# Kernel optimization log

Measured on AMD Instinct MI355X. Metric: run time of the kernel, lower is better.

## Reference

```python
import jax, jax.numpy as jnp
import numpy as np

NUM_SUB = 2  # top-k experts kept by the gate


def setup_inputs() -> dict:
    key = jax.random.key(0)
    kx, kr, kw = jax.random.split(key, 3)
    B, C, H, W, E = 16, 256, 64, 64, 8
    inputs = jax.random.normal(kx, (B, C, H, W), dtype=jnp.float32)
    W_router = jax.random.normal(kr, (C, E), dtype=jnp.float32) / np.sqrt(C)
    b_router = jnp.zeros((E,), dtype=jnp.float32)
    W_exp = jax.random.normal(kw, (E, C, C), dtype=jnp.float32) / np.sqrt(C)
    b_exp = jnp.zeros((E, C), dtype=jnp.float32)
    return {"inputs": inputs, "W_router": W_router, "b_router": b_router,
            "W_exp": W_exp, "b_exp": b_exp, "k": 2}


def reference(inputs, W_router, b_router, W_exp, b_exp, k):
    # Router: global-avg-pool + linear -> [B, E]
    E = W_router.shape[1]
    pooled = inputs.mean(axis=(2, 3))                       # [B, C]
    logits = pooled @ W_router + b_router                   # [B, E]
    # softmax in fp32 then cast back (matches F.softmax(..., dtype=torch.float))
    weights = jax.nn.softmax(logits.astype(jnp.float32), axis=1).astype(inputs.dtype)
    # top-k gating: scatter of gathered values == weights * topk-mask
    _, topk_idx = jax.lax.top_k(weights, NUM_SUB)            # [B, k]
    mask = jax.nn.one_hot(topk_idx, E, dtype=weights.dtype).sum(axis=1)  # [B, E]
    exp_w = weights * mask                                   # sparse gates [B, E]
    # out = inputs + sum_e gate[b,e] * (conv1x1_e(inputs))
    # expert weight W_exp[e, d, c]: out_d = sum_c W[d,c] x_c + b_d
    out = inputs \
        + jnp.einsum('be,edc,bchw->bdhw', exp_w, W_exp, inputs) \
        + jnp.einsum('be,ed->bd', exp_w, b_exp)[:, :, None, None]
    return out
```

## Files before the change

kernel.cpp:

```cpp
#include <hip/hip_runtime.h>
#include <hip/hip_bf16.h>

typedef __bf16 bf16x8 __attribute__((ext_vector_type(8)));
typedef float f32x4 __attribute__((ext_vector_type(4)));
typedef unsigned short ushort4v __attribute__((ext_vector_type(4)));
typedef unsigned short ushort8v __attribute__((ext_vector_type(8)));

#define B_  16
#define C_  256
#define HW_ 4096
#define E_  8

__device__ inline unsigned short f2bf(float f) {
    unsigned int b = __builtin_bit_cast(unsigned int, f);
    b += 0x7FFFu + ((b >> 16) & 1u);
    return (unsigned short)(b >> 16);
}

__global__ __launch_bounds__(256) void k_pool(const float* __restrict__ in,
                                              float* __restrict__ pooled) {
    int bc = blockIdx.x;
    const float* p = in + (size_t)bc * HW_;
    int t = threadIdx.x;
    float s = 0.f;
#pragma unroll
    for (int i = 0; i < 4; i++) {
        float4 v = *reinterpret_cast<const float4*>(p + (size_t)(t + i * 256) * 4);
        s += v.x + v.y + v.z + v.w;
    }
#pragma unroll
    for (int off = 32; off; off >>= 1) s += __shfl_down(s, off, 64);
    __shared__ float part[4];
    if ((t & 63) == 0) part[t >> 6] = s;
    __syncthreads();
    if (t == 0) pooled[bc] = (part[0] + part[1] + part[2] + part[3]) * (1.0f / HW_);
}

__global__ __launch_bounds__(256) void k_wg(const float* __restrict__ pooled,
                                            const float* __restrict__ Wr,
                                            const float* __restrict__ br,
                                            const float* __restrict__ Wexp,
                                            const float* __restrict__ bexp,
                                            unsigned short* __restrict__ Weff,
                                            float* __restrict__ biasE) {
    __shared__ float pooledS[C_];
    __shared__ float wrs[C_ * E_];
    __shared__ float lgp[64];
    __shared__ float gL[E_];
    const int t = threadIdx.x;
    const int b = blockIdx.y, dblk = blockIdx.x;

    pooledS[t] = pooled[b * C_ + t];
#pragma unroll
    for (int i = 0; i < 2; ++i)
        reinterpret_cast<float4*>(wrs)[t + i * 256] =
            reinterpret_cast<const float4*>(Wr)[t + i * 256];
    __syncthreads();
    if (t < 64) {
        const int e = t & 7, seg = t >> 3;
        float s = 0.f;
#pragma unroll
        for (int c = seg * 32; c < seg * 32 + 32; ++c)
            s += pooledS[c] * wrs[c * E_ + e];
        lgp[t] = s;
    }
    __syncthreads();
    if (t == 0) {
        float w[E_];
        float m = -1e30f;
#pragma unroll
        for (int e = 0; e < E_; ++e) {
            float s = br[e];
#pragma unroll
            for (int k = 0; k < 8; ++k) s += lgp[k * 8 + e];
            w[e] = s; m = fmaxf(m, s);
        }
        float sum = 0.f;
#pragma unroll
        for (int e = 0; e < E_; ++e) { w[e] = __expf(w[e] - m); sum += w[e]; }
        float inv = 1.f / sum;
#pragma unroll
        for (int e = 0; e < E_; ++e) w[e] *= inv;
        int i0 = 0;
#pragma unroll
        for (int e = 1; e < E_; ++e) if (w[e] > w[i0]) i0 = e;
        int i1 = -1;
#pragma unroll
        for (int e = 0; e < E_; ++e) {
            if (e == i0) continue;
            if (i1 < 0 || w[e] > w[i1]) i1 = e;
        }
#pragma unroll
        for (int e = 0; e < E_; ++e)
            gL[e] = (e == i0 || e == i1) ? w[e] : 0.f;
    }
    __syncthreads();
    if (dblk == 0) {
        float s = 0.f;
#pragma unroll
        for (int e = 0; e < E_; ++e) s += gL[e] * bexp[e * C_ + t];
        biasE[b * C_ + t] = s;
    }
    const int dloc = t >> 5, cq = t & 31;
    const int d = dblk * 8 + dloc;
#pragma unroll
    for (int half = 0; half < 2; half++) {
        const int c = (cq + half * 32) * 4;
        float4 a = {0.f, 0.f, 0.f, 0.f};
#pragma unroll
        for (int e = 0; e < E_; e++) {
            float ge = gL[e];
            if (ge != 0.f) {
                float4 wv = *reinterpret_cast<const float4*>(
                    Wexp + ((size_t)(e * C_ + d)) * C_ + c);
                a.x += ge * wv.x; a.y += ge * wv.y;
                a.z += ge * wv.z; a.w += ge * wv.w;
            }
        }
        const int diff = d - c;
        if (diff == 0) a.x += 1.f;
        else if (diff == 1) a.y += 1.f;
        else if (diff == 2) a.z += 1.f;
        else if (diff == 3) a.w += 1.f;
        ushort4v o = { f2bf(a.x), f2bf(a.y), f2bf(a.z), f2bf(a.w) };
        *reinterpret_cast<ushort4v*>(Weff + ((size_t)(b * C_ + d)) * C_ + c) = o;
    }
}

__global__ __launch_bounds__(512, 8) void k_fused(const float* __restrict__ in,
                                                  const unsigned short* __restrict__ Weff,
                                                  const float* __restrict__ biasE,
                                                  float* __restrict__ out) {
    __shared__ unsigned short Bs[64 * 256];
    __shared__ float biasS[C_];

    const int t  = threadIdx.x;
    const int b  = blockIdx.y;
    const int n0 = blockIdx.x * 64;
    const int lane = t & 63, w = t >> 6;
    const int kg = lane >> 4, lr = lane & 15;
    const float* Xb = in + ((size_t)b * C_) * HW_ + n0;
    const unsigned short* Ab = Weff + (size_t)b * C_ * C_;

    if (t < C_) biasS[t] = biasE[b * C_ + t];

    {
        const int dc = (lane >> 4) * 2;
        const int pl = (lane & 15) * 2;
#pragma unroll
        for (int it = 0; it < 8; ++it) {
            const int u = it * 8 + w;
            const int c_oct  = u & 31;
            const int p_half = u >> 5;
            const int c = c_oct * 8 + dc;
            const int p = p_half * 32 + pl;
            const float* s = Xb + (size_t)c * HW_ + p;
            float2 v0 = *reinterpret_cast<const float2*>(s);
            float2 v1 = *reinterpret_cast<const float2*>(s + HW_);
            unsigned int ue = (unsigned int)f2bf(v0.x) | ((unsigned int)f2bf(v1.x) << 16);
            unsigned int uo = (unsigned int)f2bf(v0.y) | ((unsigned int)f2bf(v1.y) << 16);
            const int cse = c_oct ^ (p & 7);
            const int cso = c_oct ^ ((p + 1) & 7);
            *reinterpret_cast<unsigned int*>(&Bs[p * 256 + cse * 8 + dc]) = ue;
            *reinterpret_cast<unsigned int*>(&Bs[(p + 1) * 256 + cso * 8 + dc]) = uo;
        }
    }
    __syncthreads();

    f32x4 acc[2][4];
#pragma unroll
    for (int fd = 0; fd < 2; ++fd) {
        const float bias = biasS[w * 32 + fd * 16 + lr];
#pragma unroll
        for (int pf = 0; pf < 4; ++pf)
            acc[fd][pf] = (f32x4){bias, bias, bias, bias};
    }

#pragma unroll
    for (int kf = 0; kf < 8; ++kf) {
        bf16x8 wf[2];
#pragma unroll
        for (int fd = 0; fd < 2; ++fd) {
            const int row = w * 32 + fd * 16 + lr;
            wf[fd] = __builtin_bit_cast(bf16x8,
                *reinterpret_cast<const ushort8v*>(
                    &Ab[(size_t)row * C_ + kf * 32 + kg * 8]));
        }
#pragma unroll
        for (int pf = 0; pf < 4; ++pf) {
            const int p = pf * 16 + lr;
            const int cc = (kf * 4 + kg) ^ (p & 7);
            bf16x8 xf = __builtin_bit_cast(bf16x8,
                *reinterpret_cast<const ushort8v*>(&Bs[p * 256 + cc * 8]));
            acc[0][pf] = __builtin_amdgcn_mfma_f32_16x16x32_bf16(
                xf, wf[0], acc[0][pf], 0, 0, 0);
            acc[1][pf] = __builtin_amdgcn_mfma_f32_16x16x32_bf16(
                xf, wf[1], acc[1][pf], 0, 0, 0);
        }
    }

    float* outB = out + ((size_t)b * C_) * HW_ + n0;
#pragma unroll
    for (int fd = 0; fd < 2; ++fd) {
        const int row = w * 32 + fd * 16 + lr;
        float* orow = outB + (size_t)row * HW_;
#pragma unroll
        for (int pf = 0; pf < 4; ++pf) {
            *reinterpret_cast<f32x4*>(&orow[pf * 16 + kg * 4]) = acc[fd][pf];
        }
    }
}

extern "C" void kernel_launch(void* const* d_in, const int* in_sizes, int n_in,
                              void* d_out, int out_size, void* d_ws, size_t ws_size,
                              hipStream_t stream) {
    const float* in   = (const float*)d_in[0];
    const float* Wr   = (const float*)d_in[1];
    const float* br   = (const float*)d_in[2];
    const float* Wexp = (const float*)d_in[3];
    const float* bexp = (const float*)d_in[4];
    float* out = (float*)d_out;
    char* ws = (char*)d_ws;

    float* pooled         = (float*)(ws);
    float* biasE          = (float*)(ws + 0x11000);
    unsigned short* Weff  = (unsigned short*)(ws + 0x20000);

    hipLaunchKernelGGL(k_pool,  dim3(B_ * C_), dim3(256), 0, stream, in, pooled);
    hipLaunchKernelGGL(k_wg,    dim3(32, B_),  dim3(256), 0, stream,
                       pooled, Wr, br, Wexp, bexp, Weff, biasE);
    hipLaunchKernelGGL(k_fused, dim3(HW_ / 64, B_), dim3(512), 0, stream,
                       in, Weff, biasE, out);
}
```

Measured before the change: 53.24 us.

## Fuse pooling with bf16 transpose-convert pass and read pretransposed input in GEMM

Replaces the separate pooling kernel with a prep kernel that reads the fp32 input once, computes per-tile partial channel sums, and writes a swizzled bf16 transposed copy of the input to workspace. The router kernel reduces those partials, and the GEMM kernel reads bf16 fragments directly from global memory instead of re-reading fp32 input and staging it through LDS. This removes the second full fp32 input read, at the cost of writing and re-reading an extra bf16 buffer (half the input size) and losing LDS staging in the GEMM.

Result: slower. 67.23 us (+26.3%).

```diff
diff --git a/kernel.cpp b/kernel.cpp
--- a/kernel.cpp
+++ b/kernel.cpp
@@ -17,26 +17,60 @@
     return (unsigned short)(b >> 16);
 }
 
-__global__ __launch_bounds__(256) void k_pool(const float* __restrict__ in,
-                                              float* __restrict__ pooled) {
-    int bc = blockIdx.x;
-    const float* p = in + (size_t)bc * HW_;
-    int t = threadIdx.x;
-    float s = 0.f;
-#pragma unroll
-    for (int i = 0; i < 4; i++) {
-        float4 v = *reinterpret_cast<const float4*>(p + (size_t)(t + i * 256) * 4);
-        s += v.x + v.y + v.z + v.w;
-    }
-#pragma unroll
-    for (int off = 32; off; off >>= 1) s += __shfl_down(s, off, 64);
-    __shared__ float part[4];
-    if ((t & 63) == 0) part[t >> 6] = s;
-    __syncthreads();
-    if (t == 0) pooled[bc] = (part[0] + part[1] + part[2] + part[3]) * (1.0f / HW_);
-}
-
-__global__ __launch_bounds__(256) void k_wg(const float* __restrict__ pooled,
+__global__ __launch_bounds__(512, 4) void k_prep(const float* __restrict__ in,
+                                                 float* __restrict__ partial,
+                                                 unsigned short* __restrict__ Xt) {
+    __shared__ unsigned short Bs[64 * 256];
+    __shared__ float partS[C_][2];
+    const int t  = threadIdx.x;
+    const int pt = blockIdx.x;
+    const int b  = blockIdx.y;
+    const int p0 = pt * 64;
+    const int lane = t & 63, w = t >> 6;
+    const float* Xb = in + ((size_t)b * C_) * HW_ + p0;
+
+    const int dc = (lane >> 4) * 2;
+    const int pl = (lane & 15) * 2;
+#pragma unroll
+    for (int it = 0; it < 8; ++it) {
+        const int u = it * 8 + w;
+        const int c_oct  = u & 31;
+        const int p_half = u >> 5;
+        const int c = c_oct * 8 + dc;
+        const int p = p_half * 32 + pl;
+        const float* s = Xb + (size_t)c * HW_ + p;
+        float2 v0 = *reinterpret_cast<const float2*>(s);
+        float2 v1 = *reinterpret_cast<const float2*>(s + HW_);
+        unsigned int ue = (unsigned int)f2bf(v0.x) | ((unsigned int)f2bf(v1.x) << 16);
+        unsigned int uo = (unsigned int)f2bf(v0.y) | ((unsigned int)f2bf(v1.y) << 16);
+        const int cse = c_oct ^ (p & 7);
+        const int cso = c_oct ^ ((p + 1) & 7);
+        *reinterpret_cast<unsigned int*>(&Bs[p * 256 + cse * 8 + dc]) = ue;
+        *reinterpret_cast<unsigned int*>(&Bs[(p + 1) * 256 + cso * 8 + dc]) = uo;
+        float s0 = v0.x + v0.y;
+        float s1 = v1.x + v1.y;
+        s0 += __shfl_xor(s0, 1, 64); s1 += __shfl_xor(s1, 1, 64);
+        s0 += __shfl_xor(s0, 2, 64); s1 += __shfl_xor(s1, 2, 64);
+        s0 += __shfl_xor(s0, 4, 64); s1 += __shfl_xor(s1, 4, 64);
+        s0 += __shfl_xor(s0, 8, 64); s1 += __shfl_xor(s1, 8, 64);
+        if ((lane & 15) == 0) {
+            partS[c][p_half]     = s0;
+            partS[c + 1][p_half] = s1;
+        }
+    }
+    __syncthreads();
+    if (t < C_)
+        partial[(size_t)(b * C_ + t) * 64 + pt] = partS[t][0] + partS[t][1];
+    unsigned short* dst = Xt + ((size_t)(b * HW_ + p0)) * C_;
+#pragma unroll
+    for (int i = 0; i < 4; ++i) {
+        const int off = i * 4096 + t * 8;
+        *reinterpret_cast<ushort8v*>(dst + off) =
+            *reinterpret_cast<const ushort8v*>(Bs + off);
+    }
+}
+
+__global__ __launch_bounds__(256) void k_wg(const float* __restrict__ partial,
                                             const float* __restrict__ Wr,
                                             const float* __restrict__ br,
                                             const float* __restrict__ Wexp,
@@ -50,7 +84,17 @@
     const int t = threadIdx.x;
     const int b = blockIdx.y, dblk = blockIdx.x;
 
-    pooledS[t] = pooled[b * C_ + t];
+    {
+        const float4* p4 = reinterpret_cast<const float4*>(
+            partial + (size_t)(b * C_ + t) * 64);
+        float s = 0.f;
+#pragma unroll
+        for (int j = 0; j < 16; ++j) {
+            float4 v = p4[j];
+            s += v.x + v.y + v.z + v.w;
+        }
+        pooledS[t] = s * (1.0f / HW_);
+    }
 #pragma unroll
     for (int i = 0; i < 2; ++i)
         reinterpret_cast<float4*>(wrs)[t + i * 256] =
@@ -127,50 +171,23 @@
     }
 }
 
-__global__ __launch_bounds__(512, 8) void k_fused(const float* __restrict__ in,
-                                                  const unsigned short* __restrict__ Weff,
-                                                  const float* __restrict__ biasE,
-                                                  float* __restrict__ out) {
-    __shared__ unsigned short Bs[64 * 256];
-    __shared__ float biasS[C_];
-
+__global__ __launch_bounds__(512, 8) void k_gemm(const unsigned short* __restrict__ Xt,
+                                                 const unsigned short* __restrict__ Weff,
+                                                 const float* __restrict__ biasE,
+                                                 float* __restrict__ out) {
     const int t  = threadIdx.x;
+    const int pt = blockIdx.x;
     const int b  = blockIdx.y;
-    const int n0 = blockIdx.x * 64;
+    const int n0 = pt * 64;
     const int lane = t & 63, w = t >> 6;
     const int kg = lane >> 4, lr = lane & 15;
-    const float* Xb = in + ((size_t)b * C_) * HW_ + n0;
-    const unsigned short* Ab = Weff + (size_t)b * C_ * C_;
-
-    if (t < C_) biasS[t] = biasE[b * C_ + t];
-
-    {
-        const int dc = (lane >> 4) * 2;
-        const int pl = (lane & 15) * 2;
-#pragma unroll
-        for (int it = 0; it < 8; ++it) {
-            const int u = it * 8 + w;
-            const int c_oct  = u & 31;
-            const int p_half = u >> 5;
-            const int c = c_oct * 8 + dc;
-            const int p = p_half * 32 + pl;
-            const float* s = Xb + (size_t)c * HW_ + p;
-            float2 v0 = *reinterpret_cast<const float2*>(s);
-            float2 v1 = *reinterpret_cast<const float2*>(s + HW_);
-            unsigned int ue = (unsigned int)f2bf(v0.x) | ((unsigned int)f2bf(v1.x) << 16);
-            unsigned int uo = (unsigned int)f2bf(v0.y) | ((unsigned int)f2bf(v1.y) << 16);
-            const int cse = c_oct ^ (p & 7);
-            const int cso = c_oct ^ ((p + 1) & 7);
-            *reinterpret_cast<unsigned int*>(&Bs[p * 256 + cse * 8 + dc]) = ue;
-            *reinterpret_cast<unsigned int*>(&Bs[(p + 1) * 256 + cso * 8 + dc]) = uo;
-        }
-    }
-    __syncthreads();
+    const unsigned short* Ab  = Weff + (size_t)b * C_ * C_;
+    const unsigned short* Xtb = Xt + ((size_t)(b * HW_ + n0)) * C_;
 
     f32x4 acc[2][4];
 #pragma unroll
     for (int fd = 0; fd < 2; ++fd) {
-        const float bias = biasS[w * 32 + fd * 16 + lr];
+        const float bias = biasE[b * C_ + w * 32 + fd * 16 + lr];
 #pragma unroll
         for (int pf = 0; pf < 4; ++pf)
             acc[fd][pf] = (f32x4){bias, bias, bias, bias};
@@ -191,7 +208,7 @@
             const int p = pf * 16 + lr;
             const int cc = (kf * 4 + kg) ^ (p & 7);
             bf16x8 xf = __builtin_bit_cast(bf16x8,
-                *reinterpret_cast<const ushort8v*>(&Bs[p * 256 + cc * 8]));
+                *reinterpret_cast<const ushort8v*>(&Xtb[p * 256 + cc * 8]));
             acc[0][pf] = __builtin_amdgcn_mfma_f32_16x16x32_bf16(
                 xf, wf[0], acc[0][pf], 0, 0, 0);
             acc[1][pf] = __builtin_amdgcn_mfma_f32_16x16x32_bf16(
@@ -222,13 +239,14 @@
     float* out = (float*)d_out;
     char* ws = (char*)d_ws;
 
-    float* pooled         = (float*)(ws);
-    float* biasE          = (float*)(ws + 0x11000);
-    unsigned short* Weff  = (unsigned short*)(ws + 0x20000);
-
-    hipLaunchKernelGGL(k_pool,  dim3(B_ * C_), dim3(256), 0, stream, in, pooled);
-    hipLaunchKernelGGL(k_wg,    dim3(32, B_),  dim3(256), 0, stream,
-                       pooled, Wr, br, Wexp, bexp, Weff, biasE);
-    hipLaunchKernelGGL(k_fused, dim3(HW_ / 64, B_), dim3(512), 0, stream,
-                       in, Weff, biasE, out);
-}
+    float* partial        = (float*)(ws);
+    unsigned short* Weff  = (unsigned short*)(ws + 0x100000);
+    float* biasE          = (float*)(ws + 0x300000);
+    unsigned short* Xt    = (unsigned short*)(ws + 0x310000);
+
+    hipLaunchKernelGGL(k_prep, dim3(64, B_), dim3(512), 0, stream, in, partial, Xt);
+    hipLaunchKernelGGL(k_wg,   dim3(32, B_), dim3(256), 0, stream,
+                       partial, Wr, br, Wexp, bexp, Weff, biasE);
+    hipLaunchKernelGGL(k_gemm, dim3(64, B_), dim3(512), 0, stream,
+                       Xt, Weff, biasE, out);
+}
```
